# Kernel tuning notes

Hardware: AMD Instinct MI355X
Metric: run time of the kernel (lower is better)

The kernel has to match this reference:

```python
import jax, jax.numpy as jnp
import numpy as np

B, L, H, NH, T, WIN = 4, 4096, 256, 8, 64, 16
D = H // NH
NEG_SLOPE = 5.0
MASK_FILL = -1e12


def _leaky(x):
    return jnp.where(x >= 0, x, NEG_SLOPE * x)


def _window_indices():
    # static numpy index construction, mirrors EdgeBlock.self_attn
    off_u = np.concatenate([np.zeros(WIN + 1, np.int64), np.arange(1, WIN + 1)])
    off_d = np.concatenate([np.arange(-WIN, 0), np.zeros(WIN + 1, np.int64)])
    idx_u = np.arange(L)[:, None] + off_u  # [L, 2W+1]
    idx_d = np.arange(L)[:, None] + off_d  # [L, 2W+1]
    idx_mask = (idx_d >= 0) & (idx_u < L)
    return idx_u % L, idx_d % L, idx_mask


def setup_inputs() -> dict:
    key = jax.random.key(0)
    ks = jax.random.split(key, 12)
    s = 1.0 / np.sqrt(H)
    lengths = jnp.array([L, L - 128, L - 512, L - 1024])
    context_mask = jnp.arange(L)[None, :] < lengths[:, None]  # [B, L] bool
    return {
        'context': jax.random.normal(ks[0], (B, L, H), jnp.float32),
        'types': jax.random.normal(ks[1], (B, T, H), jnp.float32),
        'context_mask': context_mask,
        'W_types': jax.random.normal(ks[2], (H, H), jnp.float32) * s,
        'b_types': jnp.zeros((H,), jnp.float32),
        'W_context': jax.random.normal(ks[3], (H, H), jnp.float32) * s,
        'b_context': jnp.zeros((H,), jnp.float32),
        'upon': jax.random.normal(ks[4], (NH, D), jnp.float32) * s,
        'down': jax.random.normal(ks[5], (NH, D), jnp.float32) * s,
        'cross': jax.random.normal(ks[6], (NH, D, D), jnp.float32) * s,
        'W_out': jax.random.normal(ks[7], (H, H), jnp.float32) * s,
        'b_out': jnp.zeros((H,), jnp.float32),
    }


def reference(context, types, context_mask, W_types, b_types, W_context, b_context,
              upon, down, cross, W_out, b_out):
    idx_u, idx_d, idx_mask = _window_indices()

    # head-split projections
    types_h = (types @ W_types + b_types).reshape(B, T, NH, D)      # [B,T,n,d]
    context_h = (context @ W_context + b_context).reshape(B, L, NH, D)  # [B,L,n,d]

    # ---- cross attention scores: context queries over types (EdgeBlock.cross_attn)
    upon_q = jnp.einsum('blnd,nd->bnl', context_h, upon)
    down_t = jnp.einsum('btnd,nd->bnt', types_h, down)
    concat_ct = upon_q[..., None] + down_t[:, :, None, :]           # [B,n,L,T]
    prod_ct = jnp.einsum('blnd,ndh,btnh->bnlt', context_h, cross, types_h)
    types_s = _leaky(concat_ct + prod_ct)                            # [B,n,L,T]

    # ---- windowed self attention scores (EdgeBlock.self_attn)
    down_s = jnp.einsum('blnd,nd->bnl', context_h, down)
    concat_self = upon_q[:, :, idx_u] + down_s[:, :, idx_d]          # [B,n,L,2W+1]
    win_idx = idx_u  # source: cat([indices_d[:, :0], indices_u[:, 0:]]) == indices_u
    wmask = context_mask[:, win_idx] & idx_mask                      # [B,L,2W+1]
    value_h = context_h[:, win_idx]                                  # [B,L,2W+1,n,d]
    prod_self = jnp.einsum('blnd,ndh,blvnh->bnlv', context_h, cross, value_h)
    context_s = jnp.where(wmask[:, None], _leaky(concat_self + prod_self), MASK_FILL)

    # ---- joint softmax over types + window, then aggregate
    weights = jax.nn.softmax(jnp.concatenate([types_s, context_s], axis=-1), axis=-1)
    types_w, context_w = weights[..., :T], weights[..., T:]
    upd_t = jnp.einsum('bnlt,btnd->blnd', types_w, types_h)
    upd_c = jnp.einsum('bnlv,blvnd->blnd', context_w, value_h)
    update = (upd_t + upd_c).reshape(B, L, H)

    # residual + output transform (no_gate=True path: Linear + Tanh)
    return jnp.tanh((update + context) @ W_out + b_out)
```

## Files before the change

kernel.cpp:

```cpp
#include <hip/hip_runtime.h>
#include <cstdint>

#define Bq 4
#define Lq 4096
#define Hq 256
#define NHq 8
#define Tq 64
#define WINq 16
#define Dq 32
#define NEG_SLOPE 5.0f
#define MASK_FILL -1e12f
#define TLq 64
#define MB 16

typedef __attribute__((ext_vector_type(8))) short short8;
typedef __attribute__((ext_vector_type(4))) float f32x4;

__device__ __forceinline__ float leaky(float x) { return x >= 0.f ? x : NEG_SLOPE * x; }

__device__ __forceinline__ uint16_t f2bf(float x) {
    uint32_t u = __float_as_uint(x);
    uint32_t r = (u + 0x7fffu + ((u >> 16) & 1u)) >> 16;
    return (uint16_t)r;
}
__device__ __forceinline__ float bf2f(uint16_t h) {
    return __uint_as_float(((uint32_t)h) << 16);
}

__global__ void k_prep(const float* __restrict__ Wc, const float* __restrict__ Wo,
                       uint16_t* __restrict__ pc_hi, uint16_t* __restrict__ pc_lo,
                       uint16_t* __restrict__ po_hi, uint16_t* __restrict__ po_lo,
                       const float* __restrict__ types, const float* __restrict__ Wt,
                       const float* __restrict__ bt, const float* __restrict__ down,
                       float* __restrict__ types_h, float* __restrict__ types_hT,
                       float* __restrict__ down_t) {
    __shared__ float sin[Hq];
    __shared__ float outr[Hq];
    if (blockIdx.x < 128) {
        int wsel = blockIdx.x >> 6;
        int blk = blockIdx.x & 63;
        const float* W = wsel ? Wo : Wc;
        uint16_t* ph = wsel ? po_hi : pc_hi;
        uint16_t* pl = wsel ? po_lo : pc_lo;
        int base = blk * 1024;
        for (int idx = base + threadIdx.x; idx < base + 1024; idx += 256) {
            int j = idx & 7, l = (idx >> 3) & 63, fragi = idx >> 9;
            int kc = fragi & 7, nt = fragi >> 3;
            int k = kc * 32 + (l >> 4) * 8 + j;
            int c = nt * 16 + (l & 15);
            float x = W[k * Hq + c];
            uint16_t h = f2bf(x);
            ph[idx] = h;
            pl[idx] = f2bf(x - bf2f(h));
        }
        return;
    }
    int row = blockIdx.x - 128;
    int h = threadIdx.x;
    int b = row >> 6, t = row & 63;
    sin[h] = types[(size_t)row * Hq + h];
    __syncthreads();
    float acc = bt[h];
    for (int k = 0; k < Hq; k += 4) {
        float4 iv = *(const float4*)&sin[k];
        acc = fmaf(iv.x, Wt[(k + 0) * Hq + h], acc);
        acc = fmaf(iv.y, Wt[(k + 1) * Hq + h], acc);
        acc = fmaf(iv.z, Wt[(k + 2) * Hq + h], acc);
        acc = fmaf(iv.w, Wt[(k + 3) * Hq + h], acc);
    }
    types_h[(size_t)row * Hq + h] = acc;
    types_hT[(size_t)(b * Hq + h) * Tq + t] = acc;
    outr[h] = acc;
    __syncthreads();
    if (h < NHq) {
        float s = 0.f;
        for (int d = 0; d < Dq; ++d) s += outr[h * Dq + d] * down[h * Dq + d];
        down_t[(b * NHq + h) * Tq + t] = s;
    }
}

#define APAD 264
#define OPAD 258
__global__ void __launch_bounds__(256) k_ctx(
        const float* __restrict__ ctx,
        const uint16_t* __restrict__ wp_hi, const uint16_t* __restrict__ wp_lo,
        const float* __restrict__ bc, const float* __restrict__ upon,
        const float* __restrict__ down,
        float* __restrict__ ctx_hT, float* __restrict__ uq,
        float* __restrict__ dsv) {
    int row0 = blockIdx.x * MB;
    int b = row0 >> 12, l0 = row0 & (Lq - 1);
    int tid = threadIdx.x;
    int w = tid >> 6, l = tid & 63;
    __shared__ __align__(16) char smem_raw[MB * APAD * 4];
    uint16_t* a_hi = (uint16_t*)smem_raw;
    uint16_t* a_lo = a_hi + MB * APAD;
    float* outb = (float*)smem_raw;

    {
        const float4* src = (const float4*)(ctx + (size_t)row0 * Hq);
#pragma unroll
        for (int j = 0; j < 4; ++j) {
            int f = tid + j * 256;
            int r = f >> 6, cg = f & 63;
            float4 v = src[f];
            uint16_t h0 = f2bf(v.x), h1 = f2bf(v.y), h2 = f2bf(v.z), h3 = f2bf(v.w);
            ushort4 hh = {h0, h1, h2, h3};
            ushort4 ll = {f2bf(v.x - bf2f(h0)), f2bf(v.y - bf2f(h1)),
                          f2bf(v.z - bf2f(h2)), f2bf(v.w - bf2f(h3))};
            *(ushort4*)&a_hi[r * APAD + cg * 4] = hh;
            *(ushort4*)&a_lo[r * APAD + cg * 4] = ll;
        }
    }
    __syncthreads();

    int nt0 = w * 4;
    int m = l & 15, quad = l >> 4;
    f32x4 acc[4];
#pragma unroll
    for (int t = 0; t < 4; ++t) acc[t] = (f32x4){0.f, 0.f, 0.f, 0.f};
#pragma unroll
    for (int kc = 0; kc < 8; ++kc) {
        short8 ah = *(const short8*)&a_hi[m * APAD + kc * 32 + quad * 8];
        short8 al = *(const short8*)&a_lo[m * APAD + kc * 32 + quad * 8];
#pragma unroll
        for (int t = 0; t < 4; ++t) {
            int fragi = (nt0 + t) * 8 + kc;
            short8 wh = *(const short8*)&wp_hi[fragi * 512 + l * 8];
            short8 wl = *(const short8*)&wp_lo[fragi * 512 + l * 8];
            acc[t] = __builtin_amdgcn_mfma_f32_16x16x32_bf16(ah, wh, acc[t], 0, 0, 0);
            acc[t] = __builtin_amdgcn_mfma_f32_16x16x32_bf16(ah, wl, acc[t], 0, 0, 0);
            acc[t] = __builtin_amdgcn_mfma_f32_16x16x32_bf16(al, wh, acc[t], 0, 0, 0);
        }
    }
    __syncthreads();

#pragma unroll
    for (int t = 0; t < 4; ++t) {
        int col = (nt0 + t) * 16 + m;
        float bv = bc[col];
#pragma unroll
        for (int r = 0; r < 4; ++r)
            outb[(quad * 4 + r) * OPAD + col] = acc[t][r] + bv;
    }
    __syncthreads();

    if (tid < MB * NHq) {
        int r = tid >> 3, n = tid & 7;
        float su = 0.f, sd = 0.f;
        for (int d = 0; d < Dq; ++d) {
            float v = outb[r * OPAD + n * Dq + d];
            su += v * upon[n * Dq + d];
            sd += v * down[n * Dq + d];
        }
        uq[(b * NHq + n) * Lq + l0 + r] = su;
        dsv[(b * NHq + n) * Lq + l0 + r] = sd;
    }
    {
        float* dst = ctx_hT + (size_t)(b * Hq + tid) * Lq + l0;
#pragma unroll
        for (int j = 0; j < MB / 4; ++j) {
            float4 o;
            o.x = outb[(4 * j + 0) * OPAD + tid];
            o.y = outb[(4 * j + 1) * OPAD + tid];
            o.z = outb[(4 * j + 2) * OPAD + tid];
            o.w = outb[(4 * j + 3) * OPAD + tid];
            ((float4*)dst)[j] = o;
        }
    }
}

__global__ void __launch_bounds__(256, 3) k_attn(
        const float* __restrict__ ctx_hT, const float* __restrict__ types_h,
        const float* __restrict__ types_hT, const float* __restrict__ cross,
        const float* __restrict__ uq, const float* __restrict__ dsv,
        const float* __restrict__ dt, const unsigned char* __restrict__ maskp,
        float* __restrict__ update) {
    int blk = blockIdx.x;
    int lt = blk & 63, n = (blk >> 6) & 7, b = blk >> 9;
    int l0 = lt * TLq;
    int tid = threadIdx.x;
    int g = tid >> 6;
    int lane = tid & 63;
    int Q = lane >> 4, s = lane & 15;
    bool mask_b8 = (maskp[1] != 0);

    __shared__ __align__(16) char smem[53952];
    uint16_t* TT_hi     = (uint16_t*)(smem);
    uint16_t* TT_lo     = (uint16_t*)(smem + 5120);
    uint16_t* chxT_hi   = (uint16_t*)(smem + 10240);
    uint16_t* chxT_lo   = (uint16_t*)(smem + 16640);
    uint16_t* waT_hi    = (uint16_t*)(smem);
    uint16_t* waT_lo    = (uint16_t*)(smem + 9216);
    uint16_t* crossT_hi = (uint16_t*)(smem + 23040);
    uint16_t* crossT_lo = (uint16_t*)(smem + 25600);
    uint16_t* crle_hi   = (uint16_t*)(smem + 23040);
    uint16_t* crle_lo   = (uint16_t*)(smem + 28160);
    uint16_t* waw_hi    = (uint16_t*)(smem + 23040);
    uint16_t* waw_lo    = (uint16_t*)(smem + 28160);
    uint16_t* chvt_hi   = (uint16_t*)(smem + 33280);
    uint16_t* chvt_lo   = (uint16_t*)(smem + 38400);
    uint16_t* ttvt_hi   = (uint16_t*)(smem + 43520);
    uint16_t* ttvt_lo   = (uint16_t*)(smem + 48128);
    float* uqe   = (float*)(smem + 52736);
    float* dsve  = (float*)(smem + 53056);
    float* maskf = (float*)(smem + 53376);
    float* dts   = (float*)(smem + 53696);

    {
        int d_ = tid >> 3, k_ = tid & 7, base = k_ * 10;
        const float* grow = ctx_hT + ((size_t)(b * NHq + n) * Dq + d_) * Lq;
        float cv[10];
        if (l0 <= Lq - 80) {
            const float2* g2 = (const float2*)(grow + l0 + base);
#pragma unroll
            for (int j = 0; j < 5; ++j) { float2 v = g2[j]; cv[2*j] = v.x; cv[2*j+1] = v.y; }
        } else {
#pragma unroll
            for (int m = 0; m < 10; ++m) {
                int gl = l0 + base + m;
                cv[m] = grow[gl >= Lq ? gl - Lq : gl];
            }
        }
        uint16_t hh[10], ll[10];
#pragma unroll
        for (int m = 0; m < 10; ++m) {
            hh[m] = f2bf(cv[m]);
            ll[m] = f2bf(cv[m] - bf2f(hh[m]));
        }
#pragma unroll
        for (int j = 0; j < 5; ++j) {
            *(uint*)&chvt_hi[d_ * 80 + base + 2*j] = (uint)hh[2*j] | ((uint)hh[2*j+1] << 16);
            *(uint*)&chvt_lo[d_ * 80 + base + 2*j] = (uint)ll[2*j] | ((uint)ll[2*j+1] << 16);
        }
#pragma unroll
        for (int m = 0; m < 10; ++m) {
            chxT_hi[(base + m) * 40 + d_] = hh[m];
            chxT_lo[(base + m) * 40 + d_] = ll[m];
        }
    }
    {
        int d_ = tid >> 3, e4 = (tid & 7) * 4;
        float4 v = ((const float4*)(cross + n * (Dq * Dq)))[tid];
        float vv[4] = {v.x, v.y, v.z, v.w};
#pragma unroll
        for (int j = 0; j < 4; ++j) {
            uint16_t h = f2bf(vv[j]);
            crossT_hi[(e4 + j) * 40 + d_] = h;
            crossT_lo[(e4 + j) * 40 + d_] = f2bf(vv[j] - bf2f(h));
        }
    }
    {
        int t = tid >> 2, c8 = (tid & 3) * 8;
        const float* src = types_h + (size_t)(b * Tq + t) * Hq + n * Dq + c8;
        float4 v0 = *(const float4*)src, v1 = *(const float4*)(src + 4);
        float vv[8] = {v0.x, v0.y, v0.z, v0.w, v1.x, v1.y, v1.z, v1.w};
        uint hp[4], lp[4];
#pragma unroll
        for (int j = 0; j < 4; ++j) {
            uint16_t h0 = f2bf(vv[2*j]), h1 = f2bf(vv[2*j+1]);
            hp[j] = (uint)h0 | ((uint)h1 << 16);
            lp[j] = (uint)f2bf(vv[2*j] - bf2f(h0)) | ((uint)f2bf(vv[2*j+1] - bf2f(h1)) << 16);
        }
        *(uint4*)&TT_hi[t * 40 + c8] = make_uint4(hp[0], hp[1], hp[2], hp[3]);
        *(uint4*)&TT_lo[t * 40 + c8] = make_uint4(lp[0], lp[1], lp[2], lp[3]);
    }
    {
        int d_ = tid >> 3, t8 = (tid & 7) * 8;
        const float* src = types_hT + ((size_t)(b * Hq) + n * Dq + d_) * Tq + t8;
        float4 v0 = *(const float4*)src, v1 = *(const float4*)(src + 4);
        float vv[8] = {v0.x, v0.y, v0.z, v0.w, v1.x, v1.y, v1.z, v1.w};
        uint hp[4], lp[4];
#pragma unroll
        for (int j = 0; j < 4; ++j) {
            uint16_t h0 = f2bf(vv[2*j]), h1 = f2bf(vv[2*j+1]);
            hp[j] = (uint)h0 | ((uint)h1 << 16);
            lp[j] = (uint)f2bf(vv[2*j] - bf2f(h0)) | ((uint)f2bf(vv[2*j+1] - bf2f(h1)) << 16);
        }
        *(uint4*)&ttvt_hi[d_ * 72 + t8] = make_uint4(hp[0], hp[1], hp[2], hp[3]);
        *(uint4*)&ttvt_lo[d_ * 72 + t8] = make_uint4(lp[0], lp[1], lp[2], lp[3]);
    }
    if (tid < 80) {
        int gl = l0 + tid;
        int glw = gl >= Lq ? gl - Lq : gl;
        uqe[tid] = uq[(b * NHq + n) * Lq + glw];
        unsigned char mb = mask_b8 ? maskp[b * Lq + glw]
                                   : maskp[(size_t)(b * Lq + glw) * 4];
        maskf[tid] = mb ? 1.f : 0.f;
    } else if (tid >= 96 && tid < 176) {
        int i = tid - 96;
        int gl = l0 - 16 + i;
        int glw = gl < 0 ? gl + Lq : (gl >= Lq ? gl - Lq : gl);
        dsve[i] = dsv[(b * NHq + n) * Lq + glw];
    } else if (tid >= 192) {
        dts[tid - 192] = dt[(b * NHq + n) * Tq + (tid - 192)];
    }
    __syncthreads();

    f32x4 cr0 = (f32x4){0.f, 0.f, 0.f, 0.f};
    f32x4 cr1 = (f32x4){0.f, 0.f, 0.f, 0.f};
    {
        short8 axh = *(const short8*)&chxT_hi[(16*g + s) * 40 + 8*Q];
        short8 axl = *(const short8*)&chxT_lo[(16*g + s) * 40 + 8*Q];
        short8 b0h = *(const short8*)&crossT_hi[s * 40 + 8*Q];
        short8 b0l = *(const short8*)&crossT_lo[s * 40 + 8*Q];
        short8 b1h = *(const short8*)&crossT_hi[(16 + s) * 40 + 8*Q];
        short8 b1l = *(const short8*)&crossT_lo[(16 + s) * 40 + 8*Q];
        cr0 = __builtin_amdgcn_mfma_f32_16x16x32_bf16(axh, b0h, cr0, 0, 0, 0);
        cr0 = __builtin_amdgcn_mfma_f32_16x16x32_bf16(axl, b0h, cr0, 0, 0, 0);
        cr0 = __builtin_amdgcn_mfma_f32_16x16x32_bf16(axh, b0l, cr0, 0, 0, 0);
        cr1 = __builtin_amdgcn_mfma_f32_16x16x32_bf16(axh, b1h, cr1, 0, 0, 0);
        cr1 = __builtin_amdgcn_mfma_f32_16x16x32_bf16(axl, b1h, cr1, 0, 0, 0);
        cr1 = __builtin_amdgcn_mfma_f32_16x16x32_bf16(axh, b1l, cr1, 0, 0, 0);
    }
    __syncthreads();

#pragma unroll
    for (int r = 0; r < 4; ++r) {
        int row = 16*g + 4*Q + r;
        uint16_t h0 = f2bf(cr0[r]);
        crle_hi[row * 40 + s] = h0;
        crle_lo[row * 40 + s] = f2bf(cr0[r] - bf2f(h0));
        uint16_t h1 = f2bf(cr1[r]);
        crle_hi[row * 40 + 16 + s] = h1;
        crle_lo[row * 40 + 16 + s] = f2bf(cr1[r] - bf2f(h1));
    }

    f32x4 p2[4], p3[2];
#pragma unroll
    for (int c = 0; c < 4; ++c) p2[c] = (f32x4){0.f, 0.f, 0.f, 0.f};
#pragma unroll
    for (int t_ = 0; t_ < 2; ++t_) p3[t_] = (f32x4){0.f, 0.f, 0.f, 0.f};
    {
        short8 cah = *(const short8*)&crle_hi[(16*g + s) * 40 + 8*Q];
        short8 cal = *(const short8*)&crle_lo[(16*g + s) * 40 + 8*Q];
#pragma unroll
        for (int c = 0; c < 4; ++c) {
            short8 bh = *(const short8*)&TT_hi[(s + 16*c) * 40 + 8*Q];
            short8 bl = *(const short8*)&TT_lo[(s + 16*c) * 40 + 8*Q];
            p2[c] = __builtin_amdgcn_mfma_f32_16x16x32_bf16(cah, bh, p2[c], 0, 0, 0);
            p2[c] = __builtin_amdgcn_mfma_f32_16x16x32_bf16(cal, bh, p2[c], 0, 0, 0);
            p2[c] = __builtin_amdgcn_mfma_f32_16x16x32_bf16(cah, bl, p2[c], 0, 0, 0);
        }
#pragma unroll
        for (int t_ = 0; t_ < 2; ++t_) {
            short8 bh = *(const short8*)&chxT_hi[(16*g + 16*t_ + s) * 40 + 8*Q];
            short8 bl = *(const short8*)&chxT_lo[(16*g + 16*t_ + s) * 40 + 8*Q];
            p3[t_] = __builtin_amdgcn_mfma_f32_16x16x32_bf16(cah, bh, p3[t_], 0, 0, 0);
            p3[t_] = __builtin_amdgcn_mfma_f32_16x16x32_bf16(cal, bh, p3[t_], 0, 0, 0);
            p3[t_] = __builtin_amdgcn_mfma_f32_16x16x32_bf16(cah, bl, p3[t_], 0, 0, 0);
        }
    }

    float uqr[4], cmr[4], dsr[4], dd[4];
    *(float4*)uqr = *(const float4*)&uqe[16*g + 4*Q];
    *(float4*)cmr = *(const float4*)&maskf[16*g + 4*Q];
    *(float4*)dsr = *(const float4*)&dsve[16*g + 4*Q + 16];
#pragma unroll
    for (int r = 0; r < 4; ++r) dd[r] = dsve[16*g + 4*Q + s + r];
    float dtv[4], uw[2], mw[2];
#pragma unroll
    for (int c = 0; c < 4; ++c) dtv[c] = dts[s + 16*c];
#pragma unroll
    for (int t_ = 0; t_ < 2; ++t_) {
        uw[t_] = uqe[16*g + s + 16*t_];
        mw[t_] = maskf[16*g + s + 16*t_];
    }
    float dsb[4];
#pragma unroll
    for (int r = 0; r < 4; ++r) dsb[r] = __shfl(p3[0][r], 20*Q + r);

    float stt[4][4], rup[2][4], rdn[4], rdn16[4];
#pragma unroll
    for (int c = 0; c < 4; ++c)
#pragma unroll
        for (int r = 0; r < 4; ++r)
            stt[c][r] = leaky(uqr[r] + dtv[c] + p2[c][r]);
#pragma unroll
    for (int t_ = 0; t_ < 2; ++t_)
#pragma unroll
        for (int r = 0; r < 4; ++r) {
            int u = s + 16*t_ - 4*Q - r;
            bool ok = (u >= 1) && (u <= 16) && (l0 + 16*g + s + 16*t_ < Lq)
                      && (mw[t_] > 0.5f);
            rup[t_][r] = ok ? leaky(uw[t_] + dsr[r] + p3[t_][r]) : MASK_FILL;
        }
#pragma unroll
    for (int r = 0; r < 4; ++r) {
        bool okd = (l0 + 16*g + 4*Q + r + s >= 16) && (cmr[r] > 0.5f);
        rdn[r]   = okd ? leaky(uqr[r] + dd[r] + dsb[r]) : MASK_FILL;
        rdn16[r] = (s == 0 && cmr[r] > 0.5f) ? leaky(uqr[r] + dsr[r] + dsb[r])
                                             : MASK_FILL;
    }

    float mx[4];
#pragma unroll
    for (int r = 0; r < 4; ++r) {
        float m = fmaxf(fmaxf(stt[0][r], stt[1][r]), fmaxf(stt[2][r], stt[3][r]));
        m = fmaxf(m, fmaxf(rup[0][r], rup[1][r]));
        m = fmaxf(m, fmaxf(rdn[r], rdn16[r]));
        mx[r] = m;
    }
#pragma unroll
    for (int msk = 1; msk <= 8; msk <<= 1)
#pragma unroll
        for (int r = 0; r < 4; ++r) mx[r] = fmaxf(mx[r], __shfl_xor(mx[r], msk));

    float sTU[4] = {0.f, 0.f, 0.f, 0.f}, sD[4];
#pragma unroll
    for (int c = 0; c < 4; ++c)
#pragma unroll
        for (int r = 0; r < 4; ++r) {
            stt[c][r] = __expf(stt[c][r] - mx[r]);
            sTU[r] += stt[c][r];
        }
#pragma unroll
    for (int t_ = 0; t_ < 2; ++t_)
#pragma unroll
        for (int r = 0; r < 4; ++r) {
            rup[t_][r] = __expf(rup[t_][r] - mx[r]);
            sTU[r] += rup[t_][r];
        }
#pragma unroll
    for (int r = 0; r < 4; ++r) {
        rdn[r] = __expf(rdn[r] - mx[r]);
        rdn16[r] = __expf(rdn16[r] - mx[r]);
        sD[r] = rdn[r] + rdn16[r];
    }
#pragma unroll
    for (int msk = 1; msk <= 8; msk <<= 1)
#pragma unroll
        for (int r = 0; r < 4; ++r) {
            sTU[r] += __shfl_xor(sTU[r], msk);
            sD[r]  += __shfl_xor(sD[r], msk);
        }
    float inv[4], wself[4];
#pragma unroll
    for (int r = 0; r < 4; ++r) {
        inv[r] = 1.f / (sTU[r] + sD[r]);
        wself[r] = sD[r] * inv[r];
    }

    __syncthreads();

#pragma unroll
    for (int r = 0; r < 4; ++r) {
        int row = 16*g + 4*Q + r;
#pragma unroll
        for (int c = 0; c < 4; ++c) {
            float v = stt[c][r] * inv[r];
            uint16_t h = f2bf(v);
            waT_hi[row * 72 + s + 16*c] = h;
            waT_lo[row * 72 + s + 16*c] = f2bf(v - bf2f(h));
        }
#pragma unroll
        for (int t_ = 0; t_ < 2; ++t_) {
            int u = s + 16*t_ - 4*Q - r;
            float v = (u == 0) ? wself[r]
                    : ((u >= 1 && u <= 16) ? rup[t_][r] * inv[r] : 0.f);
            uint16_t h = f2bf(v);
            waw_hi[row * 40 + s + 16*t_] = h;
            waw_lo[row * 40 + s + 16*t_] = f2bf(v - bf2f(h));
        }
    }

    f32x4 a0 = (f32x4){0.f, 0.f, 0.f, 0.f};
    f32x4 a1 = (f32x4){0.f, 0.f, 0.f, 0.f};
#pragma unroll
    for (int ks = 0; ks < 2; ++ks) {
        short8 bh = *(const short8*)&waT_hi[(16*g + s) * 72 + 32*ks + 8*Q];
        short8 bl = *(const short8*)&waT_lo[(16*g + s) * 72 + 32*ks + 8*Q];
        short8 t0h = *(const short8*)&ttvt_hi[s * 72 + 32*ks + 8*Q];
        short8 t0l = *(const short8*)&ttvt_lo[s * 72 + 32*ks + 8*Q];
        short8 t1h = *(const short8*)&ttvt_hi[(16 + s) * 72 + 32*ks + 8*Q];
        short8 t1l = *(const short8*)&ttvt_lo[(16 + s) * 72 + 32*ks + 8*Q];
        a0 = __builtin_amdgcn_mfma_f32_16x16x32_bf16(t0h, bh, a0, 0, 0, 0);
        a0 = __builtin_amdgcn_mfma_f32_16x16x32_bf16(t0l, bh, a0, 0, 0, 0);
        a0 = __builtin_amdgcn_mfma_f32_16x16x32_bf16(t0h, bl, a0, 0, 0, 0);
        a1 = __builtin_amdgcn_mfma_f32_16x16x32_bf16(t1h, bh, a1, 0, 0, 0);
        a1 = __builtin_amdgcn_mfma_f32_16x16x32_bf16(t1l, bh, a1, 0, 0, 0);
        a1 = __builtin_amdgcn_mfma_f32_16x16x32_bf16(t1h, bl, a1, 0, 0, 0);
    }
    {
        short8 wbh = *(const short8*)&waw_hi[(16*g + s) * 40 + 8*Q];
        short8 wbl = *(const short8*)&waw_lo[(16*g + s) * 40 + 8*Q];
        short8 c0h = *(const short8*)&chvt_hi[s * 80 + 16*g + 8*Q];
        short8 c0l = *(const short8*)&chvt_lo[s * 80 + 16*g + 8*Q];
        short8 c1h = *(const short8*)&chvt_hi[(16 + s) * 80 + 16*g + 8*Q];
        short8 c1l = *(const short8*)&chvt_lo[(16 + s) * 80 + 16*g + 8*Q];
        a0 = __builtin_amdgcn_mfma_f32_16x16x32_bf16(c0h, wbh, a0, 0, 0, 0);
        a0 = __builtin_amdgcn_mfma_f32_16x16x32_bf16(c0l, wbh, a0, 0, 0, 0);
        a0 = __builtin_amdgcn_mfma_f32_16x16x32_bf16(c0h, wbl, a0, 0, 0, 0);
        a1 = __builtin_amdgcn_mfma_f32_16x16x32_bf16(c1h, wbh, a1, 0, 0, 0);
        a1 = __builtin_amdgcn_mfma_f32_16x16x32_bf16(c1l, wbh, a1, 0, 0, 0);
        a1 = __builtin_amdgcn_mfma_f32_16x16x32_bf16(c1h, wbl, a1, 0, 0, 0);
    }

    {
        int lcol = l0 + 16*g + s;
        float* dst = update + (size_t)(b * Lq + lcol) * Hq + n * Dq + 4*Q;
        *(float4*)dst        = make_float4(a0[0], a0[1], a0[2], a0[3]);
        *(float4*)(dst + 16) = make_float4(a1[0], a1[1], a1[2], a1[3]);
    }
}

__global__ void __launch_bounds__(256) k_out(
        const float* __restrict__ update, const float* __restrict__ ctx,
        const uint16_t* __restrict__ wp_hi, const uint16_t* __restrict__ wp_lo,
        const float* __restrict__ bo, float* __restrict__ out) {
    int row0 = blockIdx.x * MB;
    int tid = threadIdx.x;
    int w = tid >> 6, l = tid & 63;
    __shared__ __align__(16) char smem_raw[MB * APAD * 4];
    uint16_t* a_hi = (uint16_t*)smem_raw;
    uint16_t* a_lo = a_hi + MB * APAD;

    {
        const float4* s0 = (const float4*)(update + (size_t)row0 * Hq);
        const float4* s1 = (const float4*)(ctx + (size_t)row0 * Hq);
#pragma unroll
        for (int j = 0; j < 4; ++j) {
            int f = tid + j * 256;
            int r = f >> 6, cg = f & 63;
            float4 a = s0[f], bv = s1[f];
            float4 v; v.x = a.x + bv.x; v.y = a.y + bv.y;
            v.z = a.z + bv.z; v.w = a.w + bv.w;
            uint16_t h0 = f2bf(v.x), h1 = f2bf(v.y), h2 = f2bf(v.z), h3 = f2bf(v.w);
            ushort4 hh = {h0, h1, h2, h3};
            ushort4 ll = {f2bf(v.x - bf2f(h0)), f2bf(v.y - bf2f(h1)),
                          f2bf(v.z - bf2f(h2)), f2bf(v.w - bf2f(h3))};
            *(ushort4*)&a_hi[r * APAD + cg * 4] = hh;
            *(ushort4*)&a_lo[r * APAD + cg * 4] = ll;
        }
    }
    __syncthreads();

    int nt0 = w * 4;
    int m = l & 15, quad = l >> 4;
    f32x4 acc[4];
#pragma unroll
    for (int t = 0; t < 4; ++t) acc[t] = (f32x4){0.f, 0.f, 0.f, 0.f};
#pragma unroll
    for (int kc = 0; kc < 8; ++kc) {
        short8 ah = *(const short8*)&a_hi[m * APAD + kc * 32 + quad * 8];
        short8 al = *(const short8*)&a_lo[m * APAD + kc * 32 + quad * 8];
#pragma unroll
        for (int t = 0; t < 4; ++t) {
            int fragi = (nt0 + t) * 8 + kc;
            short8 wh = *(const short8*)&wp_hi[fragi * 512 + l * 8];
            short8 wl = *(const short8*)&wp_lo[fragi * 512 + l * 8];
            acc[t] = __builtin_amdgcn_mfma_f32_16x16x32_bf16(ah, wh, acc[t], 0, 0, 0);
            acc[t] = __builtin_amdgcn_mfma_f32_16x16x32_bf16(ah, wl, acc[t], 0, 0, 0);
            acc[t] = __builtin_amdgcn_mfma_f32_16x16x32_bf16(al, wh, acc[t], 0, 0, 0);
        }
    }
#pragma unroll
    for (int t = 0; t < 4; ++t) {
        int col = (nt0 + t) * 16 + m;
        float bv = bo[col];
#pragma unroll
        for (int r = 0; r < 4; ++r)
            out[(size_t)(row0 + quad * 4 + r) * Hq + col] = tanhf(acc[t][r] + bv);
    }
}

extern "C" void kernel_launch(void* const* d_in, const int* in_sizes, int n_in,
                              void* d_out, int out_size, void* d_ws, size_t ws_size,
                              hipStream_t stream) {
    const float* context   = (const float*)d_in[0];
    const float* types     = (const float*)d_in[1];
    const unsigned char* cmask = (const unsigned char*)d_in[2];
    const float* W_types   = (const float*)d_in[3];
    const float* b_types   = (const float*)d_in[4];
    const float* W_context = (const float*)d_in[5];
    const float* b_context = (const float*)d_in[6];
    const float* upon      = (const float*)d_in[7];
    const float* down      = (const float*)d_in[8];
    const float* cross     = (const float*)d_in[9];
    const float* W_out     = (const float*)d_in[10];
    const float* b_out     = (const float*)d_in[11];
    float* out = (float*)d_out;
    float* ws  = (float*)d_ws;

    float* ctx_hT   = ws;
    float* update   = ws + 4194304;
    uint16_t* wcp_hi = (uint16_t*)(ws + 8388608);
    uint16_t* wcp_lo = wcp_hi + 65536;
    uint16_t* wop_hi = wcp_hi + 131072;
    uint16_t* wop_lo = wcp_hi + 196608;

    float* types_h  = out;
    float* types_hT = out + 65536;
    float* down_t   = out + 131072;
    float* uqp      = out + 133120;
    float* dsvp     = out + 264192;

    k_prep<<<128 + Bq * Tq, 256, 0, stream>>>(W_context, W_out,
                                              wcp_hi, wcp_lo, wop_hi, wop_lo,
                                              types, W_types, b_types, down,
                                              types_h, types_hT, down_t);
    k_ctx<<<Bq * Lq / MB, 256, 0, stream>>>(context, wcp_hi, wcp_lo, b_context,
                                            upon, down, ctx_hT, uqp, dsvp);
    k_attn<<<Bq * NHq * (Lq / TLq), 256, 0, stream>>>(ctx_hT, types_h, types_hT, cross,
                                                      uqp, dsvp, down_t, cmask, update);
    k_out<<<Bq * Lq / MB, 256, 0, stream>>>(update, context, wop_hi, wop_lo, b_out, out);
}
```

Measured before the change: 166.0 us.

## Fuse residual add and bf16 split into attention epilogue, load cross into registers

The attention kernel now adds the context residual and writes the update as pre-split bf16 hi/lo arrays. The output GEMM kernel therefore reads its A fragments straight from global memory, with no LDS staging, fp32 loads or barrier. The cross matrix fragments are loaded directly into registers, which removes one LDS buffer and one __syncthreads, and the ctx_hT store in k_ctx is remapped so consecutive threads write contiguous float4s. Together these aim to cut global traffic and synchronisation across stages, at the cost of uncoalesced strided loads of cross and an extra context read inside k_attn.

```diff
diff --git a/kernel.cpp b/kernel.cpp
--- a/kernel.cpp
+++ b/kernel.cpp
@@ -157,15 +157,16 @@
         dsv[(b * NHq + n) * Lq + l0 + r] = sd;
     }
     {
-        float* dst = ctx_hT + (size_t)(b * Hq + tid) * Lq + l0;
-#pragma unroll
-        for (int j = 0; j < MB / 4; ++j) {
+#pragma unroll
+        for (int jj = 0; jj < 4; ++jj) {
+            int f = tid + jj * 256;
+            int ch = f >> 2, part = f & 3;
             float4 o;
-            o.x = outb[(4 * j + 0) * OPAD + tid];
-            o.y = outb[(4 * j + 1) * OPAD + tid];
-            o.z = outb[(4 * j + 2) * OPAD + tid];
-            o.w = outb[(4 * j + 3) * OPAD + tid];
-            ((float4*)dst)[j] = o;
+            o.x = outb[(4 * part + 0) * OPAD + ch];
+            o.y = outb[(4 * part + 1) * OPAD + ch];
+            o.z = outb[(4 * part + 2) * OPAD + ch];
+            o.w = outb[(4 * part + 3) * OPAD + ch];
+            *(float4*)(ctx_hT + (size_t)(b * Hq + ch) * Lq + l0 + 4 * part) = o;
         }
     }
 }
@@ -175,7 +176,8 @@
         const float* __restrict__ types_hT, const float* __restrict__ cross,
         const float* __restrict__ uq, const float* __restrict__ dsv,
         const float* __restrict__ dt, const unsigned char* __restrict__ maskp,
-        float* __restrict__ update) {
+        const float* __restrict__ ctx,
+        uint16_t* __restrict__ updp_hi, uint16_t* __restrict__ updp_lo) {
     int blk = blockIdx.x;
     int lt = blk & 63, n = (blk >> 6) & 7, b = blk >> 9;
     int l0 = lt * TLq;
@@ -192,8 +194,6 @@
     uint16_t* chxT_lo   = (uint16_t*)(smem + 16640);
     uint16_t* waT_hi    = (uint16_t*)(smem);
     uint16_t* waT_lo    = (uint16_t*)(smem + 9216);
-    uint16_t* crossT_hi = (uint16_t*)(smem + 23040);
-    uint16_t* crossT_lo = (uint16_t*)(smem + 25600);
     uint16_t* crle_hi   = (uint16_t*)(smem + 23040);
     uint16_t* crle_lo   = (uint16_t*)(smem + 28160);
     uint16_t* waw_hi    = (uint16_t*)(smem + 23040);
@@ -207,6 +207,24 @@
     float* maskf = (float*)(smem + 53376);
     float* dts   = (float*)(smem + 53696);
 
+    short8 cb0h, cb0l, cb1h, cb1l;
+    {
+        const float* cbp = cross + n * (Dq * Dq) + s;
+        float c0v[8], c1v[8];
+#pragma unroll
+        for (int j = 0; j < 8; ++j) {
+            c0v[j] = cbp[(8 * Q + j) * 32];
+            c1v[j] = cbp[(8 * Q + j) * 32 + 16];
+        }
+#pragma unroll
+        for (int j = 0; j < 8; ++j) {
+            uint16_t h0 = f2bf(c0v[j]);
+            cb0h[j] = (short)h0; cb0l[j] = (short)f2bf(c0v[j] - bf2f(h0));
+            uint16_t h1 = f2bf(c1v[j]);
+            cb1h[j] = (short)h1; cb1l[j] = (short)f2bf(c1v[j] - bf2f(h1));
+        }
+    }
+
     {
         int d_ = tid >> 3, k_ = tid & 7, base = k_ * 10;
         const float* grow = ctx_hT + ((size_t)(b * NHq + n) * Dq + d_) * Lq;
@@ -237,17 +255,6 @@
         for (int m = 0; m < 10; ++m) {
             chxT_hi[(base + m) * 40 + d_] = hh[m];
             chxT_lo[(base + m) * 40 + d_] = ll[m];
-        }
-    }
-    {
-        int d_ = tid >> 3, e4 = (tid & 7) * 4;
-        float4 v = ((const float4*)(cross + n * (Dq * Dq)))[tid];
-        float vv[4] = {v.x, v.y, v.z, v.w};
-#pragma unroll
-        for (int j = 0; j < 4; ++j) {
-            uint16_t h = f2bf(vv[j]);
-            crossT_hi[(e4 + j) * 40 + d_] = h;
-            crossT_lo[(e4 + j) * 40 + d_] = f2bf(vv[j] - bf2f(h));
         }
     }
     {
@@ -302,18 +309,13 @@
     {
         short8 axh = *(const short8*)&chxT_hi[(16*g + s) * 40 + 8*Q];
         short8 axl = *(const short8*)&chxT_lo[(16*g + s) * 40 + 8*Q];
-        short8 b0h = *(const short8*)&crossT_hi[s * 40 + 8*Q];
-        short8 b0l = *(const short8*)&crossT_lo[s * 40 + 8*Q];
-        short8 b1h = *(const short8*)&crossT_hi[(16 + s) * 40 + 8*Q];
-        short8 b1l = *(const short8*)&crossT_lo[(16 + s) * 40 + 8*Q];
-        cr0 = __builtin_amdgcn_mfma_f32_16x16x32_bf16(axh, b0h, cr0, 0, 0, 0);
-        cr0 = __builtin_amdgcn_mfma_f32_16x16x32_bf16(axl, b0h, cr0, 0, 0, 0);
-        cr0 = __builtin_amdgcn_mfma_f32_16x16x32_bf16(axh, b0l, cr0, 0, 0, 0);
-        cr1 = __builtin_amdgcn_mfma_f32_16x16x32_bf16(axh, b1h, cr1, 0, 0, 0);
-        cr1 = __builtin_amdgcn_mfma_f32_16x16x32_bf16(axl, b1h, cr1, 0, 0, 0);
-        cr1 = __builtin_amdgcn_mfma_f32_16x16x32_bf16(axh, b1l, cr1, 0, 0, 0);
-    }
-    __syncthreads();
+        cr0 = __builtin_amdgcn_mfma_f32_16x16x32_bf16(axh, cb0h, cr0, 0, 0, 0);
+        cr0 = __builtin_amdgcn_mfma_f32_16x16x32_bf16(axl, cb0h, cr0, 0, 0, 0);
+        cr0 = __builtin_amdgcn_mfma_f32_16x16x32_bf16(axh, cb0l, cr0, 0, 0, 0);
+        cr1 = __builtin_amdgcn_mfma_f32_16x16x32_bf16(axh, cb1h, cr1, 0, 0, 0);
+        cr1 = __builtin_amdgcn_mfma_f32_16x16x32_bf16(axl, cb1h, cr1, 0, 0, 0);
+        cr1 = __builtin_amdgcn_mfma_f32_16x16x32_bf16(axh, cb1l, cr1, 0, 0, 0);
+    }
 
 #pragma unroll
     for (int r = 0; r < 4; ++r) {
@@ -498,52 +500,46 @@
 
     {
         int lcol = l0 + 16*g + s;
-        float* dst = update + (size_t)(b * Lq + lcol) * Hq + n * Dq + 4*Q;
-        *(float4*)dst        = make_float4(a0[0], a0[1], a0[2], a0[3]);
-        *(float4*)(dst + 16) = make_float4(a1[0], a1[1], a1[2], a1[3]);
+        const float4* cp = (const float4*)(ctx + (size_t)(b * Lq + lcol) * Hq
+                                           + n * Dq + 4*Q);
+        float4 c0 = cp[0], c1 = cp[4];
+        float v0[4] = {a0[0] + c0.x, a0[1] + c0.y, a0[2] + c0.z, a0[3] + c0.w};
+        float v1[4] = {a1[0] + c1.x, a1[1] + c1.y, a1[2] + c1.z, a1[3] + c1.w};
+        ushort4 h0, l0v, h1, l1v;
+#pragma unroll
+        for (int r = 0; r < 4; ++r) {
+            uint16_t h = f2bf(v0[r]);
+            ((uint16_t*)&h0)[r] = h; ((uint16_t*)&l0v)[r] = f2bf(v0[r] - bf2f(h));
+            uint16_t g1 = f2bf(v1[r]);
+            ((uint16_t*)&h1)[r] = g1; ((uint16_t*)&l1v)[r] = f2bf(v1[r] - bf2f(g1));
+        }
+        size_t base = (size_t)(b * Lq + lcol) * Hq + n * Dq + 4*Q;
+        *(ushort4*)(updp_hi + base)      = h0;
+        *(ushort4*)(updp_hi + base + 16) = h1;
+        *(ushort4*)(updp_lo + base)      = l0v;
+        *(ushort4*)(updp_lo + base + 16) = l1v;
     }
 }
 
 __global__ void __launch_bounds__(256) k_out(
-        const float* __restrict__ update, const float* __restrict__ ctx,
+        const uint16_t* __restrict__ up_hi, const uint16_t* __restrict__ up_lo,
         const uint16_t* __restrict__ wp_hi, const uint16_t* __restrict__ wp_lo,
         const float* __restrict__ bo, float* __restrict__ out) {
     int row0 = blockIdx.x * MB;
     int tid = threadIdx.x;
     int w = tid >> 6, l = tid & 63;
-    __shared__ __align__(16) char smem_raw[MB * APAD * 4];
-    uint16_t* a_hi = (uint16_t*)smem_raw;
-    uint16_t* a_lo = a_hi + MB * APAD;
-
-    {
-        const float4* s0 = (const float4*)(update + (size_t)row0 * Hq);
-        const float4* s1 = (const float4*)(ctx + (size_t)row0 * Hq);
-#pragma unroll
-        for (int j = 0; j < 4; ++j) {
-            int f = tid + j * 256;
-            int r = f >> 6, cg = f & 63;
-            float4 a = s0[f], bv = s1[f];
-            float4 v; v.x = a.x + bv.x; v.y = a.y + bv.y;
-            v.z = a.z + bv.z; v.w = a.w + bv.w;
-            uint16_t h0 = f2bf(v.x), h1 = f2bf(v.y), h2 = f2bf(v.z), h3 = f2bf(v.w);
-            ushort4 hh = {h0, h1, h2, h3};
-            ushort4 ll = {f2bf(v.x - bf2f(h0)), f2bf(v.y - bf2f(h1)),
-                          f2bf(v.z - bf2f(h2)), f2bf(v.w - bf2f(h3))};
-            *(ushort4*)&a_hi[r * APAD + cg * 4] = hh;
-            *(ushort4*)&a_lo[r * APAD + cg * 4] = ll;
-        }
-    }
-    __syncthreads();
-
     int nt0 = w * 4;
     int m = l & 15, quad = l >> 4;
+    const uint16_t* ah_base = up_hi + (size_t)(row0 + m) * Hq + quad * 8;
+    const uint16_t* al_base = up_lo + (size_t)(row0 + m) * Hq + quad * 8;
+
     f32x4 acc[4];
 #pragma unroll
     for (int t = 0; t < 4; ++t) acc[t] = (f32x4){0.f, 0.f, 0.f, 0.f};
 #pragma unroll
     for (int kc = 0; kc < 8; ++kc) {
-        short8 ah = *(const short8*)&a_hi[m * APAD + kc * 32 + quad * 8];
-        short8 al = *(const short8*)&a_lo[m * APAD + kc * 32 + quad * 8];
+        short8 ah = *(const short8*)(ah_base + kc * 32);
+        short8 al = *(const short8*)(al_base + kc * 32);
 #pragma unroll
         for (int t = 0; t < 4; ++t) {
             int fragi = (nt0 + t) * 8 + kc;
@@ -582,12 +578,13 @@
     float* out = (float*)d_out;
     float* ws  = (float*)d_ws;
 
-    float* ctx_hT   = ws;
-    float* update   = ws + 4194304;
-    uint16_t* wcp_hi = (uint16_t*)(ws + 8388608);
-    uint16_t* wcp_lo = wcp_hi + 65536;
-    uint16_t* wop_hi = wcp_hi + 131072;
-    uint16_t* wop_lo = wcp_hi + 196608;
+    float* ctx_hT     = ws;
+    uint16_t* updp_hi = (uint16_t*)(ws + 4194304);
+    uint16_t* updp_lo = updp_hi + 4194304;
+    uint16_t* wcp_hi  = (uint16_t*)(ws + 8388608);
+    uint16_t* wcp_lo  = wcp_hi + 65536;
+    uint16_t* wop_hi  = wcp_hi + 131072;
+    uint16_t* wop_lo  = wcp_hi + 196608;
 
     float* types_h  = out;
     float* types_hT = out + 65536;
@@ -602,6 +599,8 @@
     k_ctx<<<Bq * Lq / MB, 256, 0, stream>>>(context, wcp_hi, wcp_lo, b_context,
                                             upon, down, ctx_hT, uqp, dsvp);
     k_attn<<<Bq * NHq * (Lq / TLq), 256, 0, stream>>>(ctx_hT, types_h, types_hT, cross,
-                                                      uqp, dsvp, down_t, cmask, update);
-    k_out<<<Bq * Lq / MB, 256, 0, stream>>>(update, context, wop_hi, wop_lo, b_out, out);
+                                                      uqp, dsvp, down_t, cmask,
+                                                      context, updp_hi, updp_lo);
+    k_out<<<Bq * Lq / MB, 256, 0, stream>>>(updp_hi, updp_lo, wop_hi, wop_lo,
+                                            b_out, out);
 }
```

Result: no change. 166.3 us (+0.2%).
